# Optimization experiments

Measured on AMD Instinct MI355X. Metric: run time of the kernel, lower is better.

## Reference

```python
import jax, jax.numpy as jnp
import numpy as np
from jax import lax

BOS, EOS = 62, 63
NEG_BIG = -10000.0


def setup_inputs() -> dict:
    key = jax.random.key(0)
    k_em, k_tag, k_len, k_tr = jax.random.split(key, 4)
    B, S, L = 512, 1024, 64
    emissions = jax.random.normal(k_em, (B, S, L), dtype=jnp.float32)
    tags = jax.random.randint(k_tag, (B, S), 0, 62).astype(jnp.int64)
    # valid-prefix mask from random lengths in [S//2, S]
    lengths = jax.random.randint(k_len, (B,), S // 2, S + 1)
    mask = (jnp.arange(S)[None, :] < lengths[:, None]).astype(jnp.float32)
    # transitions: uniform(-0.1, 0.1) with BOS/EOS constraints as in init_weights
    transitions = jax.random.uniform(k_tr, (L, L), minval=-0.1, maxval=0.1, dtype=jnp.float32)
    transitions = transitions.at[:, BOS].set(NEG_BIG)
    transitions = transitions.at[EOS, :].set(NEG_BIG)
    return {"emissions": emissions, "tags": tags, "mask": mask, "transitions": transitions}


def _crf_nll(emissions, tags, mask, transitions):
    B, S, L = emissions.shape
    # ----- gold-path scores -----
    first_tags = tags[:, 0]
    last_idx = (mask.sum(axis=1).astype(jnp.int32) - 1)  # (B,)
    last_tags = jnp.take_along_axis(tags, last_idx[:, None].astype(tags.dtype), axis=1)[:, 0]
    scores = transitions[BOS, first_tags]
    scores = scores + jnp.take_along_axis(emissions[:, 0], first_tags[:, None], axis=1)[:, 0]
    prev_t, cur_t = tags[:, :-1], tags[:, 1:]
    e_step = jnp.take_along_axis(emissions[:, 1:], cur_t[..., None], axis=-1)[..., 0]  # (B,S-1)
    t_step = transitions[prev_t, cur_t]  # (B,S-1)
    scores = scores + jnp.sum((e_step + t_step) * mask[:, 1:], axis=1)
    scores = scores + transitions[last_tags, EOS]
    # ----- log-partition via forward algorithm -----
    alpha0 = transitions[BOS][None, :] + emissions[:, 0]  # (B,L)
    em_t = jnp.moveaxis(emissions[:, 1:], 1, 0)  # (S-1,B,L)
    mk_t = mask[:, 1:].T  # (S-1,B)

    def step(alpha, xs):
        e_t, m_t = xs
        # alpha[b,i] + T[i,j] + e_t[b,j] -> logsumexp over i
        new = jax.nn.logsumexp(alpha[:, :, None] + transitions[None, :, :] + e_t[:, None, :], axis=1)
        return jnp.where(m_t[:, None] > 0, new, alpha), None

    alpha, _ = lax.scan(step, alpha0, (em_t, mk_t))
    partition = jax.nn.logsumexp(alpha + transitions[:, EOS][None, :], axis=1)  # (B,)
    return -jnp.sum(scores - partition)


def reference(emissions, tags, mask, transitions):
    return _crf_nll(emissions, tags, mask, transitions)
```

## Files before the change

### kernel.cpp

```cpp
#include <hip/hip_runtime.h>
#include <math.h>

#define BOS_TAG 62
#define EOS_TAG 63
#define S_LEN   1024
#define NCH     16
#define CH      64
#define WPB     1
#define LN2F    0.69314718055994530942f

typedef short  short8 __attribute__((ext_vector_type(8)));
typedef float  f32x4  __attribute__((ext_vector_type(4)));

template <int CTRL>
__device__ __forceinline__ int dpp_mov(int v) {
  return __builtin_amdgcn_update_dpp(v, v, CTRL, 0xf, 0xf, false);
}
template <int CTRL>
__device__ __forceinline__ float dpp_fmax_step(float v) {
  return fmaxf(v, __int_as_float(dpp_mov<CTRL>(__float_as_int(v))));
}
__device__ __forceinline__ float wave_fmax_all(float v) {
  v = dpp_fmax_step<0x111>(v); v = dpp_fmax_step<0x112>(v);
  v = dpp_fmax_step<0x114>(v); v = dpp_fmax_step<0x118>(v);
  v = dpp_fmax_step<0x142>(v); v = dpp_fmax_step<0x143>(v);
  return __int_as_float(__builtin_amdgcn_readlane(__float_as_int(v), 63));
}
template <int CTRL>
__device__ __forceinline__ float dpp_fadd_step(float v) {
  int t = __builtin_amdgcn_update_dpp(0, __float_as_int(v), CTRL, 0xf, 0xf, true);
  return v + __int_as_float(t);
}
__device__ __forceinline__ float wave_sum_all(float v) {
  v = dpp_fadd_step<0x111>(v); v = dpp_fadd_step<0x112>(v);
  v = dpp_fadd_step<0x114>(v); v = dpp_fadd_step<0x118>(v);
  v = dpp_fadd_step<0x142>(v); v = dpp_fadd_step<0x143>(v);
  return __int_as_float(__builtin_amdgcn_readlane(__float_as_int(v), 63));
}
__device__ __forceinline__ unsigned short f2bf(float v) {
  return (unsigned short)((__float_as_uint(v) + 0x8000u) >> 16);
}
__device__ __forceinline__ float bf2f(unsigned short u) {
  return __uint_as_float(((unsigned)u) << 16);
}

__global__ __launch_bounds__(256) void crf_prep(
    const float* __restrict__ mask, const float* __restrict__ trans,
    int* __restrict__ lens, short8* __restrict__ pfrag,
    float* __restrict__ tvf, int B)
{
  const int tid = threadIdx.x;
  const int b = blockIdx.x * 4 + (tid >> 6);
  if (b < B) {
    const int l = tid & 63;
    const float4* mb = (const float4*)(mask + (size_t)b * S_LEN);
    float s = 0.f;
#pragma unroll
    for (int i = 0; i < 4; ++i) { float4 q = mb[l + 64 * i]; s += q.x + q.y + q.z + q.w; }
    s = wave_sum_all(s);
    if (l == 0) lens[b] = max(1, min(S_LEN, (int)(s + 0.5f)));
  }
  if (blockIdx.x == 0) {
    for (int e = tid; e < 1024; e += 256) {
      int lane = e & 63, kc = (e >> 6) & 1, m = (e >> 7) & 3, dir = e >> 9;
      int g = lane >> 4, c = lane & 15;
      int out_s = 16 * m + c;
      short8 f;
#pragma unroll
      for (int j = 0; j < 8; ++j) {
        int in_s = 16 * (2 * kc + (j >> 2)) + 4 * g + (j & 3);
        float tv = dir ? trans[out_s * 64 + in_s] : trans[in_s * 64 + out_s];
        f[j] = (short)f2bf(__expf(tv));
      }
      pfrag[e] = f;
    }
    if (tid < 64) tvf[tid] = __expf(trans[tid * 64 + EOS_TAG]);
  }
}

__global__ __launch_bounds__(256, 2) void crf_chunk_mfma(
    const float* __restrict__ em, const float* __restrict__ trans,
    const int* __restrict__ lens, const short8* __restrict__ pfrag,
    unsigned short* __restrict__ Vf, unsigned short* __restrict__ Vb,
    float* __restrict__ sf, float* __restrict__ sb,
    float* __restrict__ m0a, int B)
{
  const int l  = threadIdx.x & 63;
  const int w  = blockIdx.x * 4 + (threadIdx.x >> 6);
  const int nwaves = 2 * B * WPB;
  if (w >= nwaves) return;
  const int dir  = w & 1;
  const int b    = w >> 1;
  const int half = 0;
  const float* embase = em + (size_t)b * S_LEN * 64;
  const int g = l >> 4, c = l & 15;

  const int len = lens[b];

  float m0 = 0.f;
  if (dir == 0) {
    float a0 = trans[BOS_TAG * 64 + l] + embase[l];
    m0 = wave_fmax_all(a0);
    if (l == 0) m0a[b] = m0;
  }

  unsigned short* Vout = dir ? Vb : Vf;
  float* sout = dir ? sb : sf;
  int ps = -1, pr = -1;
#pragma unroll
  for (int r = 0; r < 16; ++r) {
    int kg = half * 16 + r;
    int fs = min((kg + 1) * CH, len - 1) - (kg * CH + 1);
    if (fs < 0) {
      Vout[((size_t)b * NCH + kg) * 64 + l] = 0x3F80;
      if (l == 0) sout[b * NCH + kg] = 0.f;
    }
    if (fs >= 0 && fs < CH - 1) { ps = fs; pr = r; }
  }

  short8 Af[4][2];
#pragma unroll
  for (int m = 0; m < 4; ++m)
#pragma unroll
    for (int kc = 0; kc < 2; ++kc)
      Af[m][kc] = pfrag[((dir * 4 + m) * 2 + kc) * 64 + l];

  float d[4][4];
#pragma unroll
  for (int m = 0; m < 4; ++m)
#pragma unroll
    for (int r = 0; r < 4; ++r) d[m][r] = 1.0f;
  if (dir == 0 && c == 0) {
#pragma unroll
    for (int m = 0; m < 4; ++m) {
      float4 tq = *reinterpret_cast<const float4*>(trans + BOS_TAG * 64 + 16 * m + 4 * g);
      float4 eq = *reinterpret_cast<const float4*>(embase + 16 * m + 4 * g);
      d[m][0] = __expf(tq.x + eq.x - m0);
      d[m][1] = __expf(tq.y + eq.y - m0);
      d[m][2] = __expf(tq.z + eq.z - m0);
      d[m][3] = __expf(tq.w + eq.w - m0);
    }
  }

  int sigma = 0;
  auto renorm16 = [&]() {
    float mx = d[0][0];
#pragma unroll
    for (int m = 0; m < 4; ++m)
#pragma unroll
      for (int r = 0; r < 4; ++r) mx = fmaxf(mx, d[m][r]);
    mx = wave_fmax_all(mx);
    int e = ((__float_as_int(mx) >> 23) & 0xff) - 127;
    float s = __int_as_float((127 - e) << 23);
#pragma unroll
    for (int m = 0; m < 4; ++m)
#pragma unroll
      for (int r = 0; r < 4; ++r) d[m][r] *= s;
    sigma += e;
  };
  auto save_chain = [&](int r) {
    int kg = half * 16 + r;
    if (c == r) {
      unsigned short* dst = Vout + ((size_t)b * NCH + kg) * 64;
#pragma unroll
      for (int m = 0; m < 4; ++m) {
        uint2 val;
        val.x = (unsigned)f2bf(d[m][0]) | ((unsigned)f2bf(d[m][1]) << 16);
        val.y = (unsigned)f2bf(d[m][2]) | ((unsigned)f2bf(d[m][3]) << 16);
        *reinterpret_cast<uint2*>(dst + 16 * m + 4 * g) = val;
      }
    }
    if (l == r) sout[b * NCH + kg] = (float)sigma;
  };

  const int tb0c  = (half * 16 + c) * CH + 1;
  const int tendc = min((half * 16 + c + 1) * CH, len - 1);
  auto loadE = [&](float4* q, int tl) {
    int tr = dir ? max(tendc - tl, 0) : min(tb0c + tl, S_LEN - 1);
    const float* rowp = embase + (size_t)tr * 64 + 4 * g;
    q[0] = *reinterpret_cast<const float4*>(rowp);
    q[1] = *reinterpret_cast<const float4*>(rowp + 16);
    q[2] = *reinterpret_cast<const float4*>(rowp + 32);
    q[3] = *reinterpret_cast<const float4*>(rowp + 48);
  };

  auto mfma8 = [&](const short8& bv0, const short8& bv1, f32x4* acc) {
#pragma unroll
    for (int m = 0; m < 4; ++m) {
      f32x4 z = {0.f, 0.f, 0.f, 0.f};
      z = __builtin_amdgcn_mfma_f32_16x16x32_bf16(Af[m][0], bv0, z, 0, 0, 0);
      acc[m] = __builtin_amdgcn_mfma_f32_16x16x32_bf16(Af[m][1], bv1, z, 0, 0, 0);
    }
  };

  auto bodyF = [&](const float4* q, int tl, bool rn) {
    short8 bv0, bv1;
#pragma unroll
    for (int j = 0; j < 8; ++j) {
      bv0[j] = (short)f2bf(d[(j >> 2)][j & 3]);
      bv1[j] = (short)f2bf(d[2 + (j >> 2)][j & 3]);
    }
    f32x4 acc[4];
    mfma8(bv0, bv1, acc);
#pragma unroll
    for (int m = 0; m < 4; ++m) {
      d[m][0] = acc[m][0] * __expf(q[m].x);
      d[m][1] = acc[m][1] * __expf(q[m].y);
      d[m][2] = acc[m][2] * __expf(q[m].z);
      d[m][3] = acc[m][3] * __expf(q[m].w);
    }
    if (rn) renorm16();
    if (tl == ps) save_chain(pr);
  };
  auto bodyB = [&](const float4* q, int tl, bool rn) {
    float ex[4][4];
#pragma unroll
    for (int m = 0; m < 4; ++m) {
      ex[m][0] = __expf(q[m].x); ex[m][1] = __expf(q[m].y);
      ex[m][2] = __expf(q[m].z); ex[m][3] = __expf(q[m].w);
    }
    short8 bv0, bv1;
#pragma unroll
    for (int j = 0; j < 8; ++j) {
      bv0[j] = (short)f2bf(d[(j >> 2)][j & 3] * ex[(j >> 2)][j & 3]);
      bv1[j] = (short)f2bf(d[2 + (j >> 2)][j & 3] * ex[2 + (j >> 2)][j & 3]);
    }
    f32x4 acc[4];
    mfma8(bv0, bv1, acc);
#pragma unroll
    for (int m = 0; m < 4; ++m) {
      d[m][0] = acc[m][0]; d[m][1] = acc[m][1];
      d[m][2] = acc[m][2]; d[m][3] = acc[m][3];
    }
    if (rn) renorm16();
    if (tl == ps) save_chain(pr);
  };

  float4 p0[4], p1[4], p2[4], p3[4];
  loadE(p0, 0); loadE(p1, 1); loadE(p2, 2); loadE(p3, 3);
  if (dir == 0) {
#pragma unroll 1
    for (int t4 = 0; t4 < CH; t4 += 4) {
      bodyF(p0, t4 + 0, false); loadE(p0, t4 + 4);
      bodyF(p1, t4 + 1, false); loadE(p1, t4 + 5);
      bodyF(p2, t4 + 2, false); loadE(p2, t4 + 6);
      bodyF(p3, t4 + 3, true);  loadE(p3, t4 + 7);
    }
  } else {
#pragma unroll 1
    for (int t4 = 0; t4 < CH; t4 += 4) {
      bodyB(p0, t4 + 0, false); loadE(p0, t4 + 4);
      bodyB(p1, t4 + 1, false); loadE(p1, t4 + 5);
      bodyB(p2, t4 + 2, false); loadE(p2, t4 + 6);
      bodyB(p3, t4 + 3, true);  loadE(p3, t4 + 7);
    }
  }

  {
    int kg = half * 16 + c;
    bool full = (kg + 1) * CH <= len - 1;
    if (full) {
      unsigned short* dst = Vout + ((size_t)b * NCH + kg) * 64;
#pragma unroll
      for (int m = 0; m < 4; ++m) {
        uint2 val;
        val.x = (unsigned)f2bf(d[m][0]) | ((unsigned)f2bf(d[m][1]) << 16);
        val.y = (unsigned)f2bf(d[m][2]) | ((unsigned)f2bf(d[m][3]) << 16);
        *reinterpret_cast<uint2*>(dst + 16 * m + 4 * g) = val;
      }
    }
    if (l < 16 && (half * 16 + l + 1) * CH <= len - 1)
      sout[b * NCH + half * 16 + l] = (float)sigma;
  }
}

__global__ __launch_bounds__(256) void crf_combine(
    const float* __restrict__ em, const int* __restrict__ tags,
    const float* __restrict__ trans, const int* __restrict__ lens,
    const unsigned short* __restrict__ Vf, const unsigned short* __restrict__ Vb,
    const float* __restrict__ sf, const float* __restrict__ sb,
    const float* __restrict__ m0a, const float* __restrict__ tvf,
    float* __restrict__ term, int B)
{
  const int item = blockIdx.x * 4 + (threadIdx.x >> 6);
  if (item >= B * NCH) return;
  const int b = item / NCH, k = item - b * NCH;
  const int l = threadIdx.x & 63;
  const int len = lens[b];
  const int kb = (len >= 2) ? (len - 2) / CH : 0;

  const int* tb = tags + (size_t)b * S_LEN;
  const float* emb = em + (size_t)b * S_LEN * 64;

  float t = 0.f;
  {
    float sc = 0.f;
    int t0 = k * CH + 1 + l;
    if (t0 <= min((k + 1) * CH, len - 1)) {
      int cur = tb[t0], prev = tb[t0 - 1];
      sc = emb[(size_t)t0 * 64 + cur] + trans[prev * 64 + cur];
    }
    if (k == 0) {
      if (l == 32) sc += trans[BOS_TAG * 64 + tb[0]] + emb[tb[0]];
      if (l == 33) sc += trans[tb[len - 1] * 64 + EOS_TAG];
    }
    t -= wave_sum_all(sc);
  }

  const unsigned short* vf = Vf + ((size_t)b * NCH + k) * 64;
  if (k == 0) {
    float v0 = bf2f(vf[l]);
    if (kb == 0) {
      t += m0a[b] + LN2F * sf[b * NCH] + __logf(wave_sum_all(v0 * tvf[l]));
    } else {
      t += m0a[b] + LN2F * (sf[b * NCH] + sb[b * NCH + 1])
         + __logf(wave_sum_all(v0 * bf2f(Vb[((size_t)b * NCH + 1) * 64 + l])));
    }
  } else if (k < kb) {
    float vk = bf2f(vf[l]);
    t += LN2F * sb[b * NCH + k + 1]
       + __logf(wave_sum_all(vk * bf2f(Vb[((size_t)b * NCH + k + 1) * 64 + l])))
       - __logf(wave_sum_all(vk));
  } else if (k == kb) {
    float vk = bf2f(vf[l]);
    t += __logf(wave_sum_all(vk * tvf[l])) - __logf(wave_sum_all(vk));
  }

  if (l == 0) term[item] = t;
}

__global__ __launch_bounds__(1024) void crf_final(
    const float* __restrict__ term, float* __restrict__ out, int n)
{
  __shared__ float red[16];
  float s = 0.f;
  for (int i = threadIdx.x; i < n; i += 1024) s += term[i];
  s = wave_sum_all(s);
  const int wid = threadIdx.x >> 6;
  if ((threadIdx.x & 63) == 0) red[wid] = s;
  __syncthreads();
  if (threadIdx.x == 0) {
    float tot = 0.f;
#pragma unroll
    for (int i = 0; i < 16; ++i) tot += red[i];
    out[0] = tot;
  }
}

__global__ __launch_bounds__(64) void crf_mono(
    const float* __restrict__ em, const int* __restrict__ tags,
    const float* __restrict__ mask, const float* __restrict__ trans,
    float* __restrict__ partial)
{
  const int b = blockIdx.x;
  const int l = threadIdx.x;
  const float* emb = em + (size_t)b * S_LEN * 64;
  const float* mb = mask + (size_t)b * S_LEN;
  float lenf = 0.f;
  for (int t = l; t < S_LEN; t += 64) lenf += mb[t];
  lenf = wave_sum_all(lenf);
  const int len = max(1, min(S_LEN, (int)(lenf + 0.5f)));

  float p[64];
#pragma unroll
  for (int i = 0; i < 64; ++i) p[i] = __expf(trans[i * 64 + l]) * 0.015625f;

  const int* tb = tags + (size_t)b * S_LEN;
  float sc = 0.f;
  for (int tt = 1 + l; tt <= len - 1; tt += 64)
    sc += emb[(size_t)tt * 64 + tb[tt]] + trans[tb[tt - 1] * 64 + tb[tt]];
  sc = wave_sum_all(sc);
  sc += trans[BOS_TAG * 64 + tb[0]] + emb[tb[0]] + trans[tb[len - 1] * 64 + EOS_TAG];

  float a0 = trans[BOS_TAG * 64 + l] + emb[l];
  float m0 = wave_fmax_all(a0);
  float v = __expf(a0 - m0);
  int sigma = 0;
  for (int t = 1; t <= len - 1; ++t) {
    float E = __expf(emb[(size_t)t * 64 + l]);
    int xi = __float_as_int(v);
    float s0 = 0.f, s1 = 0.f, s2 = 0.f, s3 = 0.f;
#pragma unroll
    for (int i = 0; i < 64; i += 4) {
      s0 = fmaf(__int_as_float(__builtin_amdgcn_readlane(xi, i + 0)), p[i + 0], s0);
      s1 = fmaf(__int_as_float(__builtin_amdgcn_readlane(xi, i + 1)), p[i + 1], s1);
      s2 = fmaf(__int_as_float(__builtin_amdgcn_readlane(xi, i + 2)), p[i + 2], s2);
      s3 = fmaf(__int_as_float(__builtin_amdgcn_readlane(xi, i + 3)), p[i + 3], s3);
    }
    v = ((s0 + s1) + (s2 + s3)) * E;
    float m = wave_fmax_all(v);
    int e = ((__float_as_int(m) >> 23) & 0xff) - 127;
    sigma += e + 6;
    v *= __int_as_float((127 - e) << 23);
  }
  float tvec = __expf(trans[l * 64 + EOS_TAG]);
  float lp = m0 + LN2F * (float)sigma + __logf(wave_sum_all(v * tvec));
  if (l == 0) partial[b] = lp - sc;
}

extern "C" void kernel_launch(void* const* d_in, const int* in_sizes, int n_in,
                              void* d_out, int out_size, void* d_ws, size_t ws_size,
                              hipStream_t stream) {
  const float* em = (const float*)d_in[0];
  const int* tags = (const int*)d_in[1];
  const float* mask = (const float*)d_in[2];
  const float* trans = (const float*)d_in[3];
  float* out = (float*)d_out;

  const int B = in_sizes[1] / S_LEN;

  const size_t nSig = (size_t)B * NCH;
  const size_t nV   = (size_t)B * NCH * 64;
  const size_t need = 16384 + 64 * sizeof(float)
                    + (3 * nSig + (size_t)B) * sizeof(float)
                    + (size_t)B * sizeof(int)
                    + 2 * nV * sizeof(unsigned short);

  if (ws_size >= need) {
    short8* pfrag = (short8*)d_ws;
    float* tvf  = (float*)((char*)d_ws + 16384);
    float* sf   = tvf + 64;
    float* sb   = sf + nSig;
    float* m0a  = sb + nSig;
    float* term = m0a + B;
    int*   lens = (int*)(term + nSig);
    unsigned short* Vf = (unsigned short*)(lens + B);
    unsigned short* Vb = Vf + nV;

    crf_prep<<<(B + 3) / 4, 256, 0, stream>>>(mask, trans, lens, pfrag, tvf, B);
    const int nwaves = 2 * B * WPB;
    crf_chunk_mfma<<<(nwaves + 3) / 4, 256, 0, stream>>>(
        em, trans, lens, pfrag, Vf, Vb, sf, sb, m0a, B);
    crf_combine<<<(B * NCH + 3) / 4, 256, 0, stream>>>(
        em, tags, trans, lens, Vf, Vb, sf, sb, m0a, tvf, term, B);
    crf_final<<<1, 1024, 0, stream>>>(term, out, B * NCH);
  } else {
    float* partial = (float*)d_ws;
    crf_mono<<<B, 64, 0, stream>>>(em, tags, mask, trans, partial);
    crf_final<<<1, 1024, 0, stream>>>(partial, out, B);
  }
}
```

Before: 63.08 us.

## Switch chunked forward/backward to 32x32x16 MFMA with 32 chunks of 32 steps

Each wave now tracks 32 independent chunk chains instead of 16, using 32x32x16 bf16 MFMA on a 64x32 state split into two output halves, so each chain has 32 steps instead of 64. The transition fragments are re-laid out for the new MFMA operand format, and emission loads and state stores are reworked to match. The aim is a shorter serial dependency chain per wave and better MFMA utilisation. In exchange the combine stage handles twice as many chunk items, register pressure rises, and emission prefetch depth drops from four steps to two.

```diff
diff --git a/kernel.cpp b/kernel.cpp
--- a/kernel.cpp
+++ b/kernel.cpp
@@ -4,13 +4,12 @@
 #define BOS_TAG 62
 #define EOS_TAG 63
 #define S_LEN   1024
-#define NCH     16
-#define CH      64
-#define WPB     1
+#define NCH     32
+#define CH      32
 #define LN2F    0.69314718055994530942f
 
 typedef short  short8 __attribute__((ext_vector_type(8)));
-typedef float  f32x4  __attribute__((ext_vector_type(4)));
+typedef float  f32x16 __attribute__((ext_vector_type(16)));
 
 template <int CTRL>
 __device__ __forceinline__ int dpp_mov(int v) {
@@ -62,13 +61,14 @@
   }
   if (blockIdx.x == 0) {
     for (int e = tid; e < 1024; e += 256) {
-      int lane = e & 63, kc = (e >> 6) & 1, m = (e >> 7) & 3, dir = e >> 9;
-      int g = lane >> 4, c = lane & 15;
-      int out_s = 16 * m + c;
+      int lane = e & 63, kc = (e >> 6) & 3, t = (e >> 8) & 1, dir = e >> 9;
+      int row = lane & 31, hA = lane >> 5;
+      int a = row & 3, hp = (row >> 2) & 1, bb = row >> 3;
+      int out_s = a + 4 * t + 8 * hp + 16 * bb;
       short8 f;
 #pragma unroll
       for (int j = 0; j < 8; ++j) {
-        int in_s = 16 * (2 * kc + (j >> 2)) + 4 * g + (j & 3);
+        int in_s = 16 * kc + 8 * hA + j;
         float tv = dir ? trans[out_s * 64 + in_s] : trans[in_s * 64 + out_s];
         f[j] = (short)f2bf(__expf(tv));
       }
@@ -87,13 +87,12 @@
 {
   const int l  = threadIdx.x & 63;
   const int w  = blockIdx.x * 4 + (threadIdx.x >> 6);
-  const int nwaves = 2 * B * WPB;
+  const int nwaves = 2 * B;
   if (w >= nwaves) return;
-  const int dir  = w & 1;
-  const int b    = w >> 1;
-  const int half = 0;
+  const int dir = w & 1;
+  const int b   = w >> 1;
   const float* embase = em + (size_t)b * S_LEN * 64;
-  const int g = l >> 4, c = l & 15;
+  const int h = l >> 5, c2 = l & 31;
 
   const int len = lens[b];
 
@@ -108,169 +107,177 @@
   float* sout = dir ? sb : sf;
   int ps = -1, pr = -1;
 #pragma unroll
-  for (int r = 0; r < 16; ++r) {
-    int kg = half * 16 + r;
-    int fs = min((kg + 1) * CH, len - 1) - (kg * CH + 1);
+  for (int r = 0; r < NCH; ++r) {
+    int fs = min((r + 1) * CH, len - 1) - (r * CH + 1);
     if (fs < 0) {
-      Vout[((size_t)b * NCH + kg) * 64 + l] = 0x3F80;
-      if (l == 0) sout[b * NCH + kg] = 0.f;
+      Vout[((size_t)b * NCH + r) * 64 + l] = 0x3F80;
+      if (l == 0) sout[b * NCH + r] = 0.f;
     }
     if (fs >= 0 && fs < CH - 1) { ps = fs; pr = r; }
   }
 
-  short8 Af[4][2];
-#pragma unroll
-  for (int m = 0; m < 4; ++m)
-#pragma unroll
-    for (int kc = 0; kc < 2; ++kc)
-      Af[m][kc] = pfrag[((dir * 4 + m) * 2 + kc) * 64 + l];
-
-  float d[4][4];
-#pragma unroll
-  for (int m = 0; m < 4; ++m)
-#pragma unroll
-    for (int r = 0; r < 4; ++r) d[m][r] = 1.0f;
-  if (dir == 0 && c == 0) {
-#pragma unroll
-    for (int m = 0; m < 4; ++m) {
-      float4 tq = *reinterpret_cast<const float4*>(trans + BOS_TAG * 64 + 16 * m + 4 * g);
-      float4 eq = *reinterpret_cast<const float4*>(embase + 16 * m + 4 * g);
-      d[m][0] = __expf(tq.x + eq.x - m0);
-      d[m][1] = __expf(tq.y + eq.y - m0);
-      d[m][2] = __expf(tq.z + eq.z - m0);
-      d[m][3] = __expf(tq.w + eq.w - m0);
-    }
+  short8 Af[2][4];
+#pragma unroll
+  for (int t = 0; t < 2; ++t)
+#pragma unroll
+    for (int kc = 0; kc < 4; ++kc)
+      Af[t][kc] = pfrag[((dir * 2 + t) * 4 + kc) * 64 + l];
+
+  float d[2][16];
+#pragma unroll
+  for (int t = 0; t < 2; ++t)
+#pragma unroll
+    for (int r = 0; r < 16; ++r) d[t][r] = 1.0f;
+  if (dir == 0 && c2 == 0) {
+#pragma unroll
+    for (int bb = 0; bb < 4; ++bb)
+#pragma unroll
+      for (int t = 0; t < 2; ++t) {
+        int off = 16 * bb + 8 * h + 4 * t;
+        float4 tq = *reinterpret_cast<const float4*>(trans + BOS_TAG * 64 + off);
+        float4 eq = *reinterpret_cast<const float4*>(embase + off);
+        d[t][4 * bb + 0] = __expf(tq.x + eq.x - m0);
+        d[t][4 * bb + 1] = __expf(tq.y + eq.y - m0);
+        d[t][4 * bb + 2] = __expf(tq.z + eq.z - m0);
+        d[t][4 * bb + 3] = __expf(tq.w + eq.w - m0);
+      }
   }
 
   int sigma = 0;
-  auto renorm16 = [&]() {
+  auto renorm32 = [&]() {
     float mx = d[0][0];
 #pragma unroll
-    for (int m = 0; m < 4; ++m)
-#pragma unroll
-      for (int r = 0; r < 4; ++r) mx = fmaxf(mx, d[m][r]);
+    for (int t = 0; t < 2; ++t)
+#pragma unroll
+      for (int r = 0; r < 16; ++r) mx = fmaxf(mx, d[t][r]);
     mx = wave_fmax_all(mx);
     int e = ((__float_as_int(mx) >> 23) & 0xff) - 127;
     float s = __int_as_float((127 - e) << 23);
 #pragma unroll
-    for (int m = 0; m < 4; ++m)
-#pragma unroll
-      for (int r = 0; r < 4; ++r) d[m][r] *= s;
+    for (int t = 0; t < 2; ++t)
+#pragma unroll
+      for (int r = 0; r < 16; ++r) d[t][r] *= s;
     sigma += e;
   };
   auto save_chain = [&](int r) {
-    int kg = half * 16 + r;
-    if (c == r) {
-      unsigned short* dst = Vout + ((size_t)b * NCH + kg) * 64;
-#pragma unroll
-      for (int m = 0; m < 4; ++m) {
-        uint2 val;
-        val.x = (unsigned)f2bf(d[m][0]) | ((unsigned)f2bf(d[m][1]) << 16);
-        val.y = (unsigned)f2bf(d[m][2]) | ((unsigned)f2bf(d[m][3]) << 16);
-        *reinterpret_cast<uint2*>(dst + 16 * m + 4 * g) = val;
+    if (c2 == r) {
+      unsigned short* dst = Vout + ((size_t)b * NCH + r) * 64 + 8 * h;
+#pragma unroll
+      for (int bb = 0; bb < 4; ++bb) {
+        uint4 val;
+        val.x = (unsigned)f2bf(d[0][4 * bb + 0]) | ((unsigned)f2bf(d[0][4 * bb + 1]) << 16);
+        val.y = (unsigned)f2bf(d[0][4 * bb + 2]) | ((unsigned)f2bf(d[0][4 * bb + 3]) << 16);
+        val.z = (unsigned)f2bf(d[1][4 * bb + 0]) | ((unsigned)f2bf(d[1][4 * bb + 1]) << 16);
+        val.w = (unsigned)f2bf(d[1][4 * bb + 2]) | ((unsigned)f2bf(d[1][4 * bb + 3]) << 16);
+        *reinterpret_cast<uint4*>(dst + 16 * bb) = val;
       }
     }
-    if (l == r) sout[b * NCH + kg] = (float)sigma;
-  };
-
-  const int tb0c  = (half * 16 + c) * CH + 1;
-  const int tendc = min((half * 16 + c + 1) * CH, len - 1);
+    if (l == r) sout[b * NCH + r] = (float)sigma;
+  };
+
+  const int tb0c  = c2 * CH + 1;
+  const int tendc = min((c2 + 1) * CH, len - 1);
   auto loadE = [&](float4* q, int tl) {
     int tr = dir ? max(tendc - tl, 0) : min(tb0c + tl, S_LEN - 1);
-    const float* rowp = embase + (size_t)tr * 64 + 4 * g;
-    q[0] = *reinterpret_cast<const float4*>(rowp);
-    q[1] = *reinterpret_cast<const float4*>(rowp + 16);
-    q[2] = *reinterpret_cast<const float4*>(rowp + 32);
-    q[3] = *reinterpret_cast<const float4*>(rowp + 48);
-  };
-
-  auto mfma8 = [&](const short8& bv0, const short8& bv1, f32x4* acc) {
-#pragma unroll
-    for (int m = 0; m < 4; ++m) {
-      f32x4 z = {0.f, 0.f, 0.f, 0.f};
-      z = __builtin_amdgcn_mfma_f32_16x16x32_bf16(Af[m][0], bv0, z, 0, 0, 0);
-      acc[m] = __builtin_amdgcn_mfma_f32_16x16x32_bf16(Af[m][1], bv1, z, 0, 0, 0);
-    }
+    const float* rowp = embase + (size_t)tr * 64 + 8 * h;
+#pragma unroll
+    for (int bb = 0; bb < 4; ++bb) {
+      q[2 * bb + 0] = *reinterpret_cast<const float4*>(rowp + 16 * bb);
+      q[2 * bb + 1] = *reinterpret_cast<const float4*>(rowp + 16 * bb + 4);
+    }
+  };
+
+  auto mfma2 = [&](const short8& bv0, const short8& bv1,
+                   const short8& bv2, const short8& bv3,
+                   f32x16& a0, f32x16& a1) {
+    f32x16 z = {0.f};
+    z = __builtin_amdgcn_mfma_f32_32x32x16_bf16(Af[0][0], bv0, z, 0, 0, 0);
+    z = __builtin_amdgcn_mfma_f32_32x32x16_bf16(Af[0][1], bv1, z, 0, 0, 0);
+    z = __builtin_amdgcn_mfma_f32_32x32x16_bf16(Af[0][2], bv2, z, 0, 0, 0);
+    a0 = __builtin_amdgcn_mfma_f32_32x32x16_bf16(Af[0][3], bv3, z, 0, 0, 0);
+    f32x16 y = {0.f};
+    y = __builtin_amdgcn_mfma_f32_32x32x16_bf16(Af[1][0], bv0, y, 0, 0, 0);
+    y = __builtin_amdgcn_mfma_f32_32x32x16_bf16(Af[1][1], bv1, y, 0, 0, 0);
+    y = __builtin_amdgcn_mfma_f32_32x32x16_bf16(Af[1][2], bv2, y, 0, 0, 0);
+    a1 = __builtin_amdgcn_mfma_f32_32x32x16_bf16(Af[1][3], bv3, y, 0, 0, 0);
   };
 
   auto bodyF = [&](const float4* q, int tl, bool rn) {
-    short8 bv0, bv1;
+    short8 bv0, bv1, bv2, bv3;
 #pragma unroll
     for (int j = 0; j < 8; ++j) {
-      bv0[j] = (short)f2bf(d[(j >> 2)][j & 3]);
-      bv1[j] = (short)f2bf(d[2 + (j >> 2)][j & 3]);
-    }
-    f32x4 acc[4];
-    mfma8(bv0, bv1, acc);
-#pragma unroll
-    for (int m = 0; m < 4; ++m) {
-      d[m][0] = acc[m][0] * __expf(q[m].x);
-      d[m][1] = acc[m][1] * __expf(q[m].y);
-      d[m][2] = acc[m][2] * __expf(q[m].z);
-      d[m][3] = acc[m][3] * __expf(q[m].w);
-    }
-    if (rn) renorm16();
+      bv0[j] = (short)f2bf(d[j >> 2][0 + (j & 3)]);
+      bv1[j] = (short)f2bf(d[j >> 2][4 + (j & 3)]);
+      bv2[j] = (short)f2bf(d[j >> 2][8 + (j & 3)]);
+      bv3[j] = (short)f2bf(d[j >> 2][12 + (j & 3)]);
+    }
+    f32x16 a0, a1;
+    mfma2(bv0, bv1, bv2, bv3, a0, a1);
+#pragma unroll
+    for (int r = 0; r < 16; ++r) {
+      float e0 = __expf(((const float*)&q[(r >> 2) * 2 + 0])[r & 3]);
+      float e1 = __expf(((const float*)&q[(r >> 2) * 2 + 1])[r & 3]);
+      d[0][r] = a0[r] * e0;
+      d[1][r] = a1[r] * e1;
+    }
+    if (rn) renorm32();
     if (tl == ps) save_chain(pr);
   };
   auto bodyB = [&](const float4* q, int tl, bool rn) {
-    float ex[4][4];
-#pragma unroll
-    for (int m = 0; m < 4; ++m) {
-      ex[m][0] = __expf(q[m].x); ex[m][1] = __expf(q[m].y);
-      ex[m][2] = __expf(q[m].z); ex[m][3] = __expf(q[m].w);
-    }
-    short8 bv0, bv1;
+    short8 bv0, bv1, bv2, bv3;
 #pragma unroll
     for (int j = 0; j < 8; ++j) {
-      bv0[j] = (short)f2bf(d[(j >> 2)][j & 3] * ex[(j >> 2)][j & 3]);
-      bv1[j] = (short)f2bf(d[2 + (j >> 2)][j & 3] * ex[2 + (j >> 2)][j & 3]);
-    }
-    f32x4 acc[4];
-    mfma8(bv0, bv1, acc);
-#pragma unroll
-    for (int m = 0; m < 4; ++m) {
-      d[m][0] = acc[m][0]; d[m][1] = acc[m][1];
-      d[m][2] = acc[m][2]; d[m][3] = acc[m][3];
-    }
-    if (rn) renorm16();
+      int t = j >> 2, a = j & 3;
+      bv0[j] = (short)f2bf(d[t][0 + a]  * __expf(((const float*)&q[0 + t])[a]));
+      bv1[j] = (short)f2bf(d[t][4 + a]  * __expf(((const float*)&q[2 + t])[a]));
+      bv2[j] = (short)f2bf(d[t][8 + a]  * __expf(((const float*)&q[4 + t])[a]));
+      bv3[j] = (short)f2bf(d[t][12 + a] * __expf(((const float*)&q[6 + t])[a]));
+    }
+    f32x16 a0, a1;
+    mfma2(bv0, bv1, bv2, bv3, a0, a1);
+#pragma unroll
+    for (int r = 0; r < 16; ++r) { d[0][r] = a0[r]; d[1][r] = a1[r]; }
+    if (rn) renorm32();
     if (tl == ps) save_chain(pr);
   };
 
-  float4 p0[4], p1[4], p2[4], p3[4];
-  loadE(p0, 0); loadE(p1, 1); loadE(p2, 2); loadE(p3, 3);
+
+  float4 pA[8], pB[8];
+  loadE(pA, 0); loadE(pB, 1);
   if (dir == 0) {
 #pragma unroll 1
     for (int t4 = 0; t4 < CH; t4 += 4) {
-      bodyF(p0, t4 + 0, false); loadE(p0, t4 + 4);
-      bodyF(p1, t4 + 1, false); loadE(p1, t4 + 5);
-      bodyF(p2, t4 + 2, false); loadE(p2, t4 + 6);
-      bodyF(p3, t4 + 3, true);  loadE(p3, t4 + 7);
+      bodyF(pA, t4 + 0, false); loadE(pA, t4 + 2);
+      bodyF(pB, t4 + 1, false); loadE(pB, t4 + 3);
+      bodyF(pA, t4 + 2, false); loadE(pA, t4 + 4);
+      bodyF(pB, t4 + 3, true);  loadE(pB, t4 + 5);
     }
   } else {
 #pragma unroll 1
     for (int t4 = 0; t4 < CH; t4 += 4) {
-      bodyB(p0, t4 + 0, false); loadE(p0, t4 + 4);
-      bodyB(p1, t4 + 1, false); loadE(p1, t4 + 5);
-      bodyB(p2, t4 + 2, false); loadE(p2, t4 + 6);
-      bodyB(p3, t4 + 3, true);  loadE(p3, t4 + 7);
+      bodyB(pA, t4 + 0, false); loadE(pA, t4 + 2);
+      bodyB(pB, t4 + 1, false); loadE(pB, t4 + 3);
+      bodyB(pA, t4 + 2, false); loadE(pA, t4 + 4);
+      bodyB(pB, t4 + 3, true);  loadE(pB, t4 + 5);
     }
   }
 
   {
-    int kg = half * 16 + c;
-    bool full = (kg + 1) * CH <= len - 1;
+    bool full = (c2 + 1) * CH <= len - 1;
     if (full) {
-      unsigned short* dst = Vout + ((size_t)b * NCH + kg) * 64;
-#pragma unroll
-      for (int m = 0; m < 4; ++m) {
-        uint2 val;
-        val.x = (unsigned)f2bf(d[m][0]) | ((unsigned)f2bf(d[m][1]) << 16);
-        val.y = (unsigned)f2bf(d[m][2]) | ((unsigned)f2bf(d[m][3]) << 16);
-        *reinterpret_cast<uint2*>(dst + 16 * m + 4 * g) = val;
+      unsigned short* dst = Vout + ((size_t)b * NCH + c2) * 64 + 8 * h;
+#pragma unroll
+      for (int bb = 0; bb < 4; ++bb) {
+        uint4 val;
+        val.x = (unsigned)f2bf(d[0][4 * bb + 0]) | ((unsigned)f2bf(d[0][4 * bb + 1]) << 16);
+        val.y = (unsigned)f2bf(d[0][4 * bb + 2]) | ((unsigned)f2bf(d[0][4 * bb + 3]) << 16);
+        val.z = (unsigned)f2bf(d[1][4 * bb + 0]) | ((unsigned)f2bf(d[1][4 * bb + 1]) << 16);
+        val.w = (unsigned)f2bf(d[1][4 * bb + 2]) | ((unsigned)f2bf(d[1][4 * bb + 3]) << 16);
+        *reinterpret_cast<uint4*>(dst + 16 * bb) = val;
       }
     }
-    if (l < 16 && (half * 16 + l + 1) * CH <= len - 1)
-      sout[b * NCH + half * 16 + l] = (float)sigma;
+    if (l < NCH && (l + 1) * CH <= len - 1)
+      sout[b * NCH + l] = (float)sigma;
   }
 }
 
@@ -296,7 +303,7 @@
   {
     float sc = 0.f;
     int t0 = k * CH + 1 + l;
-    if (t0 <= min((k + 1) * CH, len - 1)) {
+    if (l < CH && t0 <= min((k + 1) * CH, len - 1)) {
       int cur = tb[t0], prev = tb[t0 - 1];
       sc = emb[(size_t)t0 * 64 + cur] + trans[prev * 64 + cur];
     }
@@ -428,7 +435,7 @@
     unsigned short* Vb = Vf + nV;
 
     crf_prep<<<(B + 3) / 4, 256, 0, stream>>>(mask, trans, lens, pfrag, tvf, B);
-    const int nwaves = 2 * B * WPB;
+    const int nwaves = 2 * B;
     crf_chunk_mfma<<<(nwaves + 3) / 4, 256, 0, stream>>>(
         em, trans, lens, pfrag, Vf, Vb, sf, sb, m0a, B);
     crf_combine<<<(B * NCH + 3) / 4, 256, 0, stream>>>(
```

Result: slower. 68.99 us (+9.4%).
